# Optimization experiments

Measured on AMD Instinct MI355X. Metric: run time of the kernel, lower is better.

## Reference

```python
import jax, jax.numpy as jnp
import numpy as np

ALPHA = 0.2  # LeakyReLU negative slope (init arg alpha)


def setup_inputs() -> dict:
    key = jax.random.key(0)
    k1, k2, k3 = jax.random.split(key, 3)
    B, N, F_in, F_out = 8, 2048, 256, 256
    inp = jax.random.normal(k1, (B, N, F_in), dtype=jnp.float32)
    adj = jnp.ones((B, N, N), dtype=jnp.float32)  # unused by the module's forward
    # xavier_uniform with gain=1.414
    gain = 1.414
    bW = gain * np.sqrt(6.0 / (F_in + F_out))
    W = jax.random.uniform(k2, (F_in, F_out), minval=-bW, maxval=bW, dtype=jnp.float32)
    ba = gain * np.sqrt(6.0 / (2 * F_out + 1))
    a = jax.random.uniform(k3, (2 * F_out, 1), minval=-ba, maxval=ba, dtype=jnp.float32)
    return {"inp": inp, "adj": adj, "W": W, "a": a}


def reference(inp, adj, W, a):
    # inp: [B, N, F_in]; W: [F_in, F_out]; a: [2*F_out, 1]. adj is unused (as in source).
    F_out = W.shape[1]
    h = jnp.matmul(inp, W)  # [B, N, F_out]
    # e[b,i,j] = leakyrelu(a1 . h_i + a2 . h_j)  (equivalent to the repeat+cat+matmul)
    a1 = a[:F_out, 0]
    a2 = a[F_out:, 0]
    s1 = jnp.einsum('bnf,f->bn', h, a1)  # [B, N]
    s2 = jnp.einsum('bnf,f->bn', h, a2)  # [B, N]
    e = jax.nn.leaky_relu(s1[:, :, None] + s2[:, None, :], negative_slope=ALPHA)  # [B, N, N]
    # global per-batch min-max normalization, then affine *30 - 20
    mn = jnp.min(e, axis=(1, 2), keepdims=True)
    mx = jnp.max(e, axis=(1, 2), keepdims=True)
    e = (e - mn) / (mx - mn) * 30.0 - 20.0
    attention = jax.nn.sigmoid(e)  # dropout p=0 / eval: identity
    h_prime = jnp.matmul(attention, h)  # [B, N, F_out]
    h_prime = jax.nn.elu(h_prime)  # concat=True branch
    return h_prime, attention
```

## Files before the change

kernel.cpp:

```cpp
#include <hip/hip_runtime.h>
#include <stdint.h>

#define B_   8
#define N_   2048
#define F_   256
#define BN_  (B_ * N_)
#define ALPHA_ 0.2f

typedef __attribute__((ext_vector_type(8))) short  short8;
typedef __attribute__((ext_vector_type(4))) float  f32x4;

__device__ __forceinline__ unsigned short f2bf(float x) {
  uint32_t u = __float_as_uint(x);
  uint32_t r = (u + 0x7fffu + ((u >> 16) & 1u)) >> 16;
  return (unsigned short)r;
}

__device__ __forceinline__ uint32_t fkey(float f) {
  uint32_t b = __float_as_uint(f);
  return b ^ (uint32_t)(((int32_t)b >> 31) | (int32_t)0x80000000);
}
__device__ __forceinline__ float ikey(uint32_t k) {
  uint32_t b = (k & 0x80000000u) ? (k ^ 0x80000000u) : ~k;
  return __uint_as_float(b);
}

__device__ __forceinline__ void async_load16(const void* g, void* l) {
  __builtin_amdgcn_global_load_lds(
      (const __attribute__((address_space(1))) uint32_t*)g,
      (__attribute__((address_space(3))) uint32_t*)l, 16, 0, 0);
}


__global__ void k_cvt_w(const float* __restrict__ W, unsigned short* __restrict__ WT2,
                        uint32_t* __restrict__ maxk, uint32_t* __restrict__ mink) {
  int k = blockIdx.x, n = threadIdx.x;
  if (k == 0 && n < 16) { maxk[n] = 0u; mink[n] = 0xFFFFFFFFu; }
  int idx = (((n >> 4) * 8 + (k >> 5)) << 9)
          + ((((k >> 3) & 3) << 4) + (n & 15)) * 8
          + (k & 7);
  WT2[idx] = f2bf(W[k * F_ + n]);
}

__launch_bounds__(256, 2)
__global__ void k_gemm1(const float* __restrict__ inp,
                        const unsigned short* __restrict__ WT2,
                        const float* __restrict__ avec,
                        unsigned short* __restrict__ hT2,
                        float* __restrict__ s1g, float* __restrict__ s2g,
                        uint32_t* __restrict__ maxk, uint32_t* __restrict__ mink) {
  __shared__ __align__(16) unsigned short Atile[64 * 32];
  __shared__ __align__(16) unsigned short Trans[256 * 72];
  __shared__ float s1_lds[64], s2_lds[64];

  const int tid  = threadIdx.x;
  const int wave = tid >> 6, lane = tid & 63;
  const int n16  = lane & 15, quad = lane >> 4;
  const int i0   = blockIdx.x * 64;
  const int b    = i0 >> 11;

  if (tid < 64) { s1_lds[tid] = 0.0f; s2_lds[tid] = 0.0f; }

  f32x4 acc[4][4];
  #pragma unroll
  for (int mt = 0; mt < 4; ++mt)
    #pragma unroll
    for (int nt = 0; nt < 4; ++nt) acc[mt][nt] = (f32x4){0.f, 0.f, 0.f, 0.f};

  const unsigned short* wbase = WT2 + (size_t)(wave * 32) * 512 + lane * 8;

  short8 bfA[4], bfB[4];
  #pragma unroll
  for (int nt = 0; nt < 4; ++nt)
    bfA[nt] = *(const short8*)(wbase + (nt * 8 + 0) * 512);

  auto body = [&](int t, short8* bfc, short8* bfn) {
    const int k0 = t << 5;
    {
      int r = tid >> 2, cp = tid & 3;
      const float* gp = inp + (size_t)(i0 + r) * F_ + k0 + cp * 8;
      float4 va = *(const float4*)gp;
      float4 vb = *(const float4*)(gp + 4);
      short8 sv;
      sv[0] = (short)f2bf(va.x); sv[1] = (short)f2bf(va.y);
      sv[2] = (short)f2bf(va.z); sv[3] = (short)f2bf(va.w);
      sv[4] = (short)f2bf(vb.x); sv[5] = (short)f2bf(vb.y);
      sv[6] = (short)f2bf(vb.z); sv[7] = (short)f2bf(vb.w);
      *(short8*)((char*)Atile + r * 64 + cp * 16) = sv;
    }
    __syncthreads();

    short8 af[4];
    #pragma unroll
    for (int mt = 0; mt < 4; ++mt)
      af[mt] = *(const short8*)((const char*)Atile + ((mt * 16 + n16) * 64 + quad * 16));

    if (t < 7) {
      #pragma unroll
      for (int nt = 0; nt < 4; ++nt)
        bfn[nt] = *(const short8*)(wbase + (nt * 8 + t + 1) * 512);
    }

    #pragma unroll
    for (int mt = 0; mt < 4; ++mt)
      #pragma unroll
      for (int nt = 0; nt < 4; ++nt)
        acc[mt][nt] = __builtin_amdgcn_mfma_f32_16x16x32_bf16(af[mt], bfc[nt], acc[mt][nt], 0, 0, 0);
    __syncthreads();
  };

  #pragma unroll
  for (int tt = 0; tt < 8; tt += 2) {
    body(tt, bfA, bfB);
    body(tt + 1, bfB, bfA);
  }

  #pragma unroll
  for (int mt = 0; mt < 4; ++mt)
    #pragma unroll
    for (int nt = 0; nt < 4; ++nt) {
      int f = (wave << 6) + (nt << 4) + n16;
      int i = (mt << 4) + (quad << 2);
      ushort4 pk;
      pk.x = f2bf(acc[mt][nt][0]); pk.y = f2bf(acc[mt][nt][1]);
      pk.z = f2bf(acc[mt][nt][2]); pk.w = f2bf(acc[mt][nt][3]);
      *(ushort4*)(Trans + f * 72 + i) = pk;
    }

  float a1v[4], a2v[4];
  #pragma unroll
  for (int nt = 0; nt < 4; ++nt) {
    int f = (wave << 6) + (nt << 4) + n16;
    a1v[nt] = avec[f];
    a2v[nt] = avec[F_ + f];
  }
  #pragma unroll
  for (int mt = 0; mt < 4; ++mt) {
    float s1p[4] = {0, 0, 0, 0}, s2p[4] = {0, 0, 0, 0};
    #pragma unroll
    for (int nt = 0; nt < 4; ++nt)
      #pragma unroll
      for (int rg = 0; rg < 4; ++rg) {
        s1p[rg] = fmaf(acc[mt][nt][rg], a1v[nt], s1p[rg]);
        s2p[rg] = fmaf(acc[mt][nt][rg], a2v[nt], s2p[rg]);
      }
    #pragma unroll
    for (int rg = 0; rg < 4; ++rg) {
      float v1 = s1p[rg], v2 = s2p[rg];
      #pragma unroll
      for (int off = 1; off < 16; off <<= 1) {
        v1 += __shfl_xor(v1, off);
        v2 += __shfl_xor(v2, off);
      }
      if (n16 == 0) {
        atomicAdd(&s1_lds[(mt << 4) + (quad << 2) + rg], v1);
        atomicAdd(&s2_lds[(mt << 4) + (quad << 2) + rg], v2);
      }
    }
  }
  __syncthreads();

  const int kb0 = (i0 & 2047) >> 5;
  #pragma unroll
  for (int p = 0; p < 8; ++p) {
    int f0  = p * 2 + (wave >> 1);
    int kbl = wave & 1;
    short8 v = *(const short8*)(Trans + (16 * f0 + (lane & 15)) * 72 + kbl * 32 + (lane >> 4) * 8);
    *(short8*)(hT2 + (size_t)((b * 16 + f0) * 64 + kb0 + kbl) * 512 + lane * 8) = v;
  }

  if (tid < 64) {
    float v1 = s1_lds[tid], v2 = s2_lds[tid];
    s1g[i0 + tid] = v1;
    s2g[i0 + tid] = v2;
    float mn1 = v1, mx1 = v1, mn2 = v2, mx2 = v2;
    #pragma unroll
    for (int off = 1; off < 64; off <<= 1) {
      mn1 = fminf(mn1, __shfl_xor(mn1, off));
      mx1 = fmaxf(mx1, __shfl_xor(mx1, off));
      mn2 = fminf(mn2, __shfl_xor(mn2, off));
      mx2 = fmaxf(mx2, __shfl_xor(mx2, off));
    }
    if (tid == 0) {
      atomicMax(&maxk[b * 2 + 0], fkey(mx1));
      atomicMax(&maxk[b * 2 + 1], fkey(mx2));
      atomicMin(&mink[b * 2 + 0], fkey(mn1));
      atomicMin(&mink[b * 2 + 1], fkey(mn2));
    }
  }
}

__launch_bounds__(256, 2)
__global__ void k_gemm2(const unsigned short* __restrict__ hT2,
                        const float* __restrict__ s1, const float* __restrict__ s2,
                        const uint32_t* __restrict__ maxk, const uint32_t* __restrict__ mink,
                        float* __restrict__ hprime,
                        float* __restrict__ att) {
  __shared__ __align__(16) char Btile[2][16384];
  __shared__ __align__(16) unsigned short Atile[2][1024];
  __shared__ __align__(16) float s2_lds[N_];

  const int tid  = threadIdx.x;
  const int wave = tid >> 6, lane = tid & 63;
  const int n16  = lane & 15, quad = lane >> 4;
  const int blk  = blockIdx.x;
  const int b    = blk & 7;
  const int i0   = (blk >> 3) * 32;

  float mx1 = ikey(maxk[b * 2 + 0]), mx2 = ikey(maxk[b * 2 + 1]);
  float mn1 = ikey(mink[b * 2 + 0]), mn2 = ikey(mink[b * 2 + 1]);
  float smn = mn1 + mn2, smx = mx1 + mx2;
  float emn = fmaxf(smn, ALPHA_ * smn);
  float emx = fmaxf(smx, ALPHA_ * smx);
  float scale  = 30.0f / (emx - emn);
  const float uscale = -scale;
  const float ubias  = emn * scale + 20.0f;

  const int r_att = tid >> 3;
  const int c_att = tid & 7;
  const float s1v = s1[b * N_ + i0 + r_att];
  const float* s2b = s2 + b * N_;
  float* attrow = att + ((size_t)(b * N_ + i0 + r_att)) * N_;

  auto stage_b = [&](int buf_, int kb) {
    #pragma unroll
    for (int g = 0; g < 4; ++g) {
      int f0 = wave * 4 + g;
      async_load16(hT2 + ((size_t)((b * 16 + f0) * 64 + kb) << 9) + lane * 8,
                   (char*)Btile + buf_ * 16384 + (f0 << 10));
    }
  };

  #pragma unroll
  for (int it = 0; it < 2; ++it)
    async_load16(s2b + wave * 512 + it * 256 + lane * 4,
                 (char*)s2_lds + wave * 2048 + it * 1024);
  stage_b(0, 0);
  asm volatile("s_waitcnt vmcnt(0) lgkmcnt(0)" ::: "memory");
  __builtin_amdgcn_s_barrier();
  asm volatile("" ::: "memory");

  f32x4 acc[2][4];
  #pragma unroll
  for (int mt = 0; mt < 2; ++mt)
    #pragma unroll
    for (int nt = 0; nt < 4; ++nt) acc[mt][nt] = (f32x4){0.f, 0.f, 0.f, 0.f};

  for (int t = 0; t < 64; ++t) {
    const int cur  = t & 1;
    const int abuf = cur * 2048;
    const int k0   = t << 5;

    float4 va = *(const float4*)((const char*)s2_lds + k0 * 4 + c_att * 16);
    float v[4] = {va.x, va.y, va.z, va.w};
    #pragma unroll
    for (int jj = 0; jj < 4; ++jj) {
      float s = s1v + v[jj];
      float l = fmaxf(s, ALPHA_ * s);
      float u = fmaf(l, uscale, ubias);
      v[jj] = __builtin_amdgcn_rcpf(1.0f + __expf(u));
    }
    *(f32x4*)(attrow + k0 + c_att * 4) = (f32x4){v[0], v[1], v[2], v[3]};
    ushort4 spk;
    spk.x = f2bf(v[0]); spk.y = f2bf(v[1]); spk.z = f2bf(v[2]); spk.w = f2bf(v[3]);
    *(ushort4*)((char*)Atile + abuf + tid * 8) = spk;

    asm volatile("s_waitcnt vmcnt(1) lgkmcnt(0)" ::: "memory");
    __builtin_amdgcn_s_barrier();
    asm volatile("" ::: "memory");

    if (t < 63) stage_b(cur ^ 1, t + 1);

    short8 af0 = *(const short8*)((const char*)Atile + abuf + n16 * 64 + quad * 16);
    short8 af1 = *(const short8*)((const char*)Atile + abuf + (16 + n16) * 64 + quad * 16);
    short8 bf_[4];
    #pragma unroll
    for (int nt = 0; nt < 4; ++nt)
      bf_[nt] = *(const short8*)((const char*)Btile + cur * 16384 +
                                 ((wave * 4 + nt) << 10) + lane * 16);

    #pragma unroll
    for (int nt = 0; nt < 4; ++nt) {
      acc[0][nt] = __builtin_amdgcn_mfma_f32_16x16x32_bf16(af0, bf_[nt], acc[0][nt], 0, 0, 0);
      acc[1][nt] = __builtin_amdgcn_mfma_f32_16x16x32_bf16(af1, bf_[nt], acc[1][nt], 0, 0, 0);
    }
  }

  float* hp = hprime + ((size_t)(b * N_ + i0)) * F_;
  #pragma unroll
  for (int mt = 0; mt < 2; ++mt)
    #pragma unroll
    for (int nt = 0; nt < 4; ++nt) {
      int fcol = (wave << 6) + (nt << 4) + n16;
      int irow = (mt << 4) + (quad << 2);
      #pragma unroll
      for (int rg = 0; rg < 4; ++rg) {
        float x = acc[mt][nt][rg];
        float y = x > 0.0f ? x : (__expf(x) - 1.0f);
        __builtin_nontemporal_store(y, hp + (size_t)(irow + rg) * F_ + fcol);
      }
    }
}

extern "C" void kernel_launch(void* const* d_in, const int* in_sizes, int n_in,
                              void* d_out, int out_size, void* d_ws, size_t ws_size,
                              hipStream_t stream) {
  const float* inp  = (const float*)d_in[0];
  const float* W    = (const float*)d_in[2];
  const float* avec = (const float*)d_in[3];

  float* hprime = (float*)d_out;
  float* att    = (float*)d_out + (size_t)B_ * N_ * F_;

  char* ws = (char*)d_ws;
  unsigned short* WT2 = (unsigned short*)ws;
  unsigned short* hT2 = (unsigned short*)(ws + 131072);
  float* s1           = (float*)(ws + 131072 + 8388608);
  float* s2           = s1 + BN_;
  uint32_t* maxk      = (uint32_t*)(s2 + BN_);
  uint32_t* mink      = maxk + 16;

  k_cvt_w<<<F_, F_, 0, stream>>>(W, WT2, maxk, mink);
  k_gemm1<<<BN_ / 64, 256, 0, stream>>>(inp, WT2, avec, hT2, s1, s2, maxk, mink);
  k_gemm2<<<512, 256, 0, stream>>>(hT2, s1, s2, maxk, mink, hprime, att);
}
```

Measured before the change: 282.8 us.

## Stage W tiles through LDS via async loads in gemm1; nontemporal attention stores

In the first GEMM, the register double-buffered global loads of W fragments are replaced by async global-to-LDS loads into a Btile region. That region shares one LDS buffer that is later reused for the transpose, which shrinks the LDS footprint. In the attention kernel, the fp32 attention matrix is written with nontemporal stores so the large output does not pollute the cache. The tradeoff is losing the register prefetch overlap of B fragments in gemm1.

```diff
diff --git a/kernel.cpp b/kernel.cpp
--- a/kernel.cpp
+++ b/kernel.cpp
@@ -29,6 +29,10 @@
   __builtin_amdgcn_global_load_lds(
       (const __attribute__((address_space(1))) uint32_t*)g,
       (__attribute__((address_space(3))) uint32_t*)l, 16, 0, 0);
+}
+
+__device__ __forceinline__ void nt_store4(float* p, f32x4 v) {
+  __builtin_nontemporal_store(v, (f32x4*)p);
 }
 
 
@@ -49,9 +53,10 @@
                         unsigned short* __restrict__ hT2,
                         float* __restrict__ s1g, float* __restrict__ s2g,
                         uint32_t* __restrict__ maxk, uint32_t* __restrict__ mink) {
-  __shared__ __align__(16) unsigned short Atile[64 * 32];
-  __shared__ __align__(16) unsigned short Trans[256 * 72];
+  __shared__ __align__(16) char smem[256 * 72 * 2];
   __shared__ float s1_lds[64], s2_lds[64];
+  unsigned short* Atile = (unsigned short*)smem;
+  char* Btile = smem + 4096;
 
   const int tid  = threadIdx.x;
   const int wave = tid >> 6, lane = tid & 63;
@@ -67,14 +72,7 @@
     #pragma unroll
     for (int nt = 0; nt < 4; ++nt) acc[mt][nt] = (f32x4){0.f, 0.f, 0.f, 0.f};
 
-  const unsigned short* wbase = WT2 + (size_t)(wave * 32) * 512 + lane * 8;
-
-  short8 bfA[4], bfB[4];
-  #pragma unroll
-  for (int nt = 0; nt < 4; ++nt)
-    bfA[nt] = *(const short8*)(wbase + (nt * 8 + 0) * 512);
-
-  auto body = [&](int t, short8* bfc, short8* bfn) {
+  for (int t = 0; t < 8; ++t) {
     const int k0 = t << 5;
     {
       int r = tid >> 2, cp = tid & 3;
@@ -88,32 +86,30 @@
       sv[6] = (short)f2bf(vb.z); sv[7] = (short)f2bf(vb.w);
       *(short8*)((char*)Atile + r * 64 + cp * 16) = sv;
     }
+    #pragma unroll
+    for (int g = 0; g < 4; ++g) {
+      int f0 = wave * 4 + g;
+      async_load16(WT2 + ((size_t)(f0 * 8 + t) << 9) + lane * 8,
+                   Btile + (f0 << 10));
+    }
     __syncthreads();
 
-    short8 af[4];
+    short8 af[4], bf_[4];
     #pragma unroll
     for (int mt = 0; mt < 4; ++mt)
       af[mt] = *(const short8*)((const char*)Atile + ((mt * 16 + n16) * 64 + quad * 16));
-
-    if (t < 7) {
-      #pragma unroll
-      for (int nt = 0; nt < 4; ++nt)
-        bfn[nt] = *(const short8*)(wbase + (nt * 8 + t + 1) * 512);
-    }
-
+    #pragma unroll
+    for (int nt = 0; nt < 4; ++nt)
+      bf_[nt] = *(const short8*)(Btile + (((wave << 2) + nt) << 10) + lane * 16);
     #pragma unroll
     for (int mt = 0; mt < 4; ++mt)
       #pragma unroll
       for (int nt = 0; nt < 4; ++nt)
-        acc[mt][nt] = __builtin_amdgcn_mfma_f32_16x16x32_bf16(af[mt], bfc[nt], acc[mt][nt], 0, 0, 0);
+        acc[mt][nt] = __builtin_amdgcn_mfma_f32_16x16x32_bf16(af[mt], bf_[nt], acc[mt][nt], 0, 0, 0);
     __syncthreads();
-  };
-
-  #pragma unroll
-  for (int tt = 0; tt < 8; tt += 2) {
-    body(tt, bfA, bfB);
-    body(tt + 1, bfB, bfA);
-  }
+  }
+
+  unsigned short* Trans = (unsigned short*)smem;
 
   #pragma unroll
   for (int mt = 0; mt < 4; ++mt)
@@ -260,7 +256,7 @@
       float u = fmaf(l, uscale, ubias);
       v[jj] = __builtin_amdgcn_rcpf(1.0f + __expf(u));
     }
-    *(f32x4*)(attrow + k0 + c_att * 4) = (f32x4){v[0], v[1], v[2], v[3]};
+    nt_store4(attrow + k0 + c_att * 4, (f32x4){v[0], v[1], v[2], v[3]});
     ushort4 spk;
     spk.x = f2bf(v[0]); spk.y = f2bf(v[1]); spk.z = f2bf(v[2]); spk.w = f2bf(v[3]);
     *(ushort4*)((char*)Atile + abuf + tid * 8) = spk;
@@ -277,7 +273,7 @@
     #pragma unroll
     for (int nt = 0; nt < 4; ++nt)
       bf_[nt] = *(const short8*)((const char*)Btile + cur * 16384 +
-                                 ((wave * 4 + nt) << 10) + lane * 16);
+                                 (((wave << 2) + nt) << 10) + lane * 16);
 
     #pragma unroll
     for (int nt = 0; nt < 4; ++nt) {
```

After: 278.1 us. No clear change (-1.7%).
